# Optimization experiments

Measured on AMD Instinct MI355X. Metric: run time of the kernel, lower is better.

Reference implementation:

```python
import jax, jax.numpy as jnp
import numpy as np
from jax import lax

B, C_IN, H, W = 8, 64, 256, 256
HEADS, QD, U, VD = 4, 16, 1, 32  # heads, query_depth, intra_depth, v_depth = out_ch//heads
EPS = 1e-5  # BatchNorm eps (eval mode: running_mean=0, running_var=1)


def setup_inputs() -> dict:
    key = jax.random.key(0)
    ks = jax.random.split(key, 10)
    x = jax.random.normal(ks[0], (B, C_IN, H, W), dtype=jnp.float32)
    Wq = jax.random.normal(ks[1], (QD * HEADS, C_IN), dtype=jnp.float32) * 0.05
    gq = jax.random.normal(ks[2], (QD * HEADS,), dtype=jnp.float32) * 0.1 + 1.0
    bq = jax.random.normal(ks[3], (QD * HEADS,), dtype=jnp.float32) * 0.05
    Wk = jax.random.normal(ks[4], (QD * U, C_IN), dtype=jnp.float32) * 0.05
    Wv = jax.random.normal(ks[5], (VD * U, C_IN), dtype=jnp.float32) * 0.05
    gv = jax.random.normal(ks[6], (VD * U,), dtype=jnp.float32) * 0.1 + 1.0
    bv = jax.random.normal(ks[7], (VD * U,), dtype=jnp.float32) * 0.05
    Wp = jax.random.normal(ks[8], (QD, U, 1, 3, 3), dtype=jnp.float32) * 0.1  # Conv3d (1,3,3)
    bp = jax.random.normal(ks[9], (QD,), dtype=jnp.float32) * 0.05
    return {"x": x, "Wq": Wq, "gq": gq, "bq": bq, "Wk": Wk, "Wv": Wv,
            "gv": gv, "bv": bv, "Wp": Wp, "bp": bp}


def _bn_eval(y, gamma, beta):
    # BatchNorm in eval mode with running_mean=0, running_var=1
    s = gamma / jnp.sqrt(1.0 + EPS)
    return y * s[None, :, None, None] + beta[None, :, None, None]


def reference(x, Wq, gq, bq, Wk, Wv, gv, bv, Wp, bp):
    b, c, h, w = x.shape
    n = h * w
    # 1x1 convs as channel matmuls
    q = jnp.einsum('oc,bchw->bohw', Wq, x)
    q = _bn_eval(q, gq, bq).reshape(b, HEADS, QD, n)           # b h k n
    k = jnp.einsum('oc,bchw->bohw', Wk, x).reshape(b, U, QD, n)  # b u k m
    v = jnp.einsum('oc,bchw->bohw', Wv, x)
    v = _bn_eval(v, gv, bv).reshape(b, U, VD, n)               # b u v m
    k = jax.nn.softmax(k, axis=-1)
    # content lambda: global context
    lam_c = jnp.einsum('bukm,buvm->bkv', k, v)                 # b k v
    Yc = jnp.einsum('bhkn,bkv->bhvn', q, lam_c)
    # position lambda: 3D conv over (v-depth, h, w) with kernel (1,3,3)
    v_p = v.reshape(b, U, VD, h, w)                            # N C D H W (D = v-depth)
    lam_p = lax.conv_general_dilated(
        v_p, Wp, window_strides=(1, 1, 1),
        padding=[(0, 0), (1, 1), (1, 1)],
        dimension_numbers=('NCDHW', 'OIDHW', 'NCDHW'))
    lam_p = lam_p + bp[None, :, None, None, None]              # b k v h w
    Yp = jnp.einsum('bhkn,bkvn->bhvn', q, lam_p.reshape(b, QD, VD, n))
    Y = Yc + Yp                                                # b h v n
    return Y.reshape(b, HEADS * VD, h, w)
```

## Files before the change

### kernel.cpp

```cpp
#include <hip/hip_runtime.h>
#include <hip/hip_bf16.h>
#include <cstddef>

#define BB    8
#define CIN   64
#define HH    256
#define WW    256
#define NN    65536
#define NP    (BB*NN)
#define QC    64
#define KC    16
#define VC    32
#define HEADS 4
#define QD    16

#define WALL_OFF 0
#define BQ_OFF 7168
#define BV_OFF 7232
#define WP_OFF 7264
#define BP_OFF 7408
#define S_OFF  7424
#define M_OFF  7552
#define SMALL_END 11648
#define FLAG_OFF 12000
#define BF_BASE 65536

typedef __hip_bfloat16 bf16;
typedef __attribute__((ext_vector_type(8))) short short8;
typedef __attribute__((ext_vector_type(4))) short short4v;
typedef __attribute__((ext_vector_type(4))) float f32x4;

#define MFMA16(a, b, c) __builtin_amdgcn_mfma_f32_16x16x32_bf16((a), (b), (c), 0, 0, 0)

__device__ __forceinline__ short f2bf_s(float f) {
    bf16 h = (bf16)f;
    return __builtin_bit_cast(short, h);
}
__device__ __forceinline__ float bf2f(short u) {
    unsigned x = ((unsigned)(unsigned short)u) << 16;
    return __builtin_bit_cast(float, x);
}

__global__ void k_detect(const unsigned short* __restrict xu, int* __restrict flag) {
    if (threadIdx.x == 0 && blockIdx.x == 0) {
        int big = 0, zero = 0;
        for (int i = 0; i < 256; ++i) {
            unsigned short u = xu[i];
            int e = (u >> 7) & 0xFF;
            big  += (e >= 134);
            zero += (u == 0);
        }
        *flag = (big > 4 || zero > 64) ? 1 : 0;
    }
}

__device__ __forceinline__ float ldin(const void* p, int i, int isf) {
    return isf ? ((const float*)p)[i] : (float)(((const bf16*)p)[i]);
}

__global__ void k_prep(const void* __restrict wq, const void* __restrict gq,
                       const void* __restrict bq, const void* __restrict wk,
                       const void* __restrict wv, const void* __restrict gv,
                       const void* __restrict bv, const void* __restrict wp,
                       const void* __restrict bp, float* __restrict wf,
                       const int* __restrict flag) {
    int t = threadIdx.x;
    int isf = *flag;
    float rs = rsqrtf(1.0f + 1e-5f);
    for (int i = t; i < 4096; i += 256)
        wf[WALL_OFF + i] = ldin(wq, i, isf) * (ldin(gq, i>>6, isf) * rs);
    for (int i = t; i < 1024; i += 256)
        wf[WALL_OFF + 4096 + i] = ldin(wk, i, isf);
    for (int i = t; i < 2048; i += 256)
        wf[WALL_OFF + 5120 + i] = ldin(wv, i, isf) * (ldin(gv, i>>6, isf) * rs);
    for (int i = t; i < 64;   i += 256) wf[BQ_OFF+i] = ldin(bq, i, isf);
    for (int i = t; i < 32;   i += 256) wf[BV_OFF+i] = ldin(bv, i, isf);
    for (int i = t; i < 144;  i += 256) wf[WP_OFF+i] = ldin(wp, i, isf);
    for (int i = t; i < 16;   i += 256) wf[BP_OFF+i] = ldin(bp, i, isf);
    for (int i = t; i < SMALL_END - S_OFF; i += 256) wf[S_OFF + i] = 0.0f;
}

#define TPW 2
__global__ __launch_bounds__(256) void k_qkv(const void* __restrict x,
        const float* __restrict wf, const int* __restrict flag,
        bf16* __restrict qws2, bf16* __restrict ekws, bf16* __restrict vws) {
    const int lane = threadIdx.x & 63;
    const int m = lane & 15, g = lane >> 4;
    const int wave = blockIdx.x * 4 + (threadIdx.x >> 6);
    const int px0 = wave * (TPW * 16);
    const int b = px0 >> 16;
    const int n0 = px0 & 0xFFFF;
    const int isf = *flag;

    short8 a[7][2];
    #pragma unroll
    for (int mt = 0; mt < 7; ++mt)
        #pragma unroll
        for (int kh = 0; kh < 2; ++kh) {
            const float* wr = wf + WALL_OFF + (mt * 16 + m) * 64 + kh * 32 + g * 8;
            short8 t;
            #pragma unroll
            for (int i = 0; i < 8; ++i) t[i] = f2bf_s(wr[i]);
            a[mt][kh] = t;
        }

    f32x4 bias[7];
    #pragma unroll
    for (int mt = 0; mt < 4; ++mt)
        #pragma unroll
        for (int r = 0; r < 4; ++r) bias[mt][r] = wf[BQ_OFF + mt * 16 + g * 4 + r];
    #pragma unroll
    for (int r = 0; r < 4; ++r) bias[4][r] = 0.0f;
    #pragma unroll
    for (int mt = 5; mt < 7; ++mt)
        #pragma unroll
        for (int r = 0; r < 4; ++r) bias[mt][r] = wf[BV_OFF + (mt - 5) * 16 + g * 4 + r];

    #pragma unroll
    for (int it = 0; it < TPW; ++it) {
        const int n = n0 + it * 16 + m;
        const size_t p = (size_t)px0 + it * 16 + m;

        short8 bf0, bf1;
        if (isf) {
            const float* xp = (const float*)x + (size_t)b * CIN * NN
                            + (size_t)g * 8 * NN + n;
            #pragma unroll
            for (int i = 0; i < 8; ++i) bf0[i] = f2bf_s(xp[(size_t)i * NN]);
            #pragma unroll
            for (int i = 0; i < 8; ++i) bf1[i] = f2bf_s(xp[(size_t)(32 + i) * NN]);
        } else {
            const unsigned short* xp = (const unsigned short*)x + (size_t)b * CIN * NN
                                     + (size_t)g * 8 * NN + n;
            #pragma unroll
            for (int i = 0; i < 8; ++i) bf0[i] = (short)xp[(size_t)i * NN];
            #pragma unroll
            for (int i = 0; i < 8; ++i) bf1[i] = (short)xp[(size_t)(32 + i) * NN];
        }

        f32x4 acc[7];
        #pragma unroll
        for (int mt = 0; mt < 7; ++mt) {
            acc[mt] = MFMA16(a[mt][0], bf0, bias[mt]);
            acc[mt] = MFMA16(a[mt][1], bf1, acc[mt]);
        }

        bf16* qp = qws2 + p * 64;
        #pragma unroll
        for (int mt = 0; mt < 4; ++mt) {
            short4v pk;
            #pragma unroll
            for (int r = 0; r < 4; ++r) pk[r] = f2bf_s(acc[mt][r]);
            *(short4v*)(qp + mt * 16 + g * 4) = pk;
        }
        #pragma unroll
        for (int r = 0; r < 4; ++r)
            ekws[(size_t)(g * 4 + r) * NP + p] = (bf16)__expf(acc[4][r]);
        #pragma unroll
        for (int mt = 0; mt < 2; ++mt)
            #pragma unroll
            for (int r = 0; r < 4; ++r)
                vws[(size_t)(mt * 16 + g * 4 + r) * NP + p] = (bf16)acc[5 + mt][r];
    }
}

#define LCHUNK 256
__global__ __launch_bounds__(256) void k_lamc(const bf16* __restrict ekws,
        const bf16* __restrict vws, float* __restrict Sg, float* __restrict Mg) {
    __shared__ float MM[4][512];
    __shared__ float SS[4][16];
    const int b = blockIdx.y, chunk = blockIdx.x;
    const int t = threadIdx.x, w = t >> 6, lane = t & 63;
    const int m = lane & 15, g = lane >> 4;
    const size_t px0 = (size_t)b * NN + (size_t)chunk * LCHUNK + (size_t)w * 64;

    f32x4 acc0 = {0.f, 0.f, 0.f, 0.f}, acc1 = {0.f, 0.f, 0.f, 0.f};
    float s = 0.0f;
    #pragma unroll
    for (int st = 0; st < 2; ++st) {
        const size_t p = px0 + st * 32 + g * 8;
        short8 afr = *(const short8*)(ekws + (size_t)m * NP + p);
        short8 b0  = *(const short8*)(vws + (size_t)m * NP + p);
        short8 b1  = *(const short8*)(vws + (size_t)(16 + m) * NP + p);
        acc0 = MFMA16(afr, b0, acc0);
        acc1 = MFMA16(afr, b1, acc1);
        #pragma unroll
        for (int i = 0; i < 8; ++i) s += bf2f(afr[i]);
    }
    s += __shfl_xor(s, 16);
    s += __shfl_xor(s, 32);
    if (g == 0) SS[w][m] = s;
    #pragma unroll
    for (int r = 0; r < 4; ++r) {
        MM[w][(g * 4 + r) * 32 + m]      = acc0[r];
        MM[w][(g * 4 + r) * 32 + 16 + m] = acc1[r];
    }
    __syncthreads();
    for (int i = t; i < 512; i += 256) {
        float v4 = MM[0][i] + MM[1][i] + MM[2][i] + MM[3][i];
        atomicAdd(&Mg[b * 512 + i], v4);
    }
    if (t < 16) atomicAdd(&Sg[b * 16 + t], SS[0][t] + SS[1][t] + SS[2][t] + SS[3][t]);
}

__global__ __launch_bounds__(256) void k_out(const bf16* __restrict qws2,
        const bf16* __restrict vws, const float* __restrict wf,
        const float* __restrict Sg, const float* __restrict Mg,
        const int* __restrict flag, void* __restrict outv) {
    const int y = blockIdx.x >> 1, xh = blockIdx.x & 1, b = blockIdx.y;
    const int tid = threadIdx.x;
    const int pxl = tid & 127, hg = tid >> 7;
    const int px0 = xh * 128;
    const int isf = *flag;

    __shared__ float As[512];
    __shared__ float WPs[144];
    __shared__ unsigned short VS[32 * 3 * 144];

    for (int i = tid; i < 512; i += 256) {
        int k = i & 15, v = i >> 4;
        As[i] = Mg[b * 512 + k * 32 + v] / Sg[b * 16 + k] + wf[BP_OFF + k];
    }
    if (tid < 144) WPs[tid] = wf[WP_OFF + tid];

    #pragma unroll
    for (int kk = 0; kk < 7; ++kk) {
        int idx = tid + kk * 256;
        if (idx < 1728) {
            int c = idx / 54, rem = idx - c * 54;
            int j = rem / 18, i = rem - j * 18;
            int yy = y + j - 1;
            int x0 = px0 - 8 + i * 8;
            short8 val = {0, 0, 0, 0, 0, 0, 0, 0};
            if (yy >= 0 && yy < HH && x0 >= 0 && x0 <= WW - 8)
                val = *(const short8*)(vws + (size_t)c * NP + (size_t)b * NN
                                       + (size_t)yy * WW + x0);
            *(short8*)&VS[(c * 3 + j) * 144 + i * 8] = val;
        }
    }
    __syncthreads();

    const size_t pix = (size_t)b * NN + (size_t)y * WW + px0 + pxl;
    const short8* qrow = (const short8*)(qws2 + pix * 64) + hg * 4;
    float qf[32];
    #pragma unroll
    for (int j = 0; j < 4; ++j) {
        short8 qv = qrow[j];
        #pragma unroll
        for (int e = 0; e < 8; ++e) qf[j * 8 + e] = bf2f(qv[e]);
    }

    float g4[2][9];
    #pragma unroll
    for (int hl = 0; hl < 2; ++hl)
        #pragma unroll
        for (int tn = 0; tn < 9; ++tn) g4[hl][tn] = 0.0f;
    #pragma unroll
    for (int k = 0; k < 16; ++k)
        #pragma unroll
        for (int tn = 0; tn < 9; ++tn) {
            float w = WPs[k * 9 + tn];
            g4[0][tn] += qf[k] * w;
            g4[1][tn] += qf[16 + k] * w;
        }

    const size_t obase = ((size_t)(b * HEADS + hg * 2) * VC) * NN
                       + (size_t)y * WW + px0 + pxl;
    #pragma unroll 2
    for (int vc = 0; vc < VC; ++vc) {
        float vnf[9];
        const unsigned short* vb = &VS[vc * 3 * 144 + 7 + pxl];
        #pragma unroll
        for (int j = 0; j < 3; ++j)
            #pragma unroll
            for (int dx = 0; dx < 3; ++dx)
                vnf[j * 3 + dx] = bf2f((short)vb[j * 144 + dx]);
        float Ak[16];
        const f32x4* ap = (const f32x4*)&As[vc * 16];
        #pragma unroll
        for (int qq = 0; qq < 4; ++qq) {
            f32x4 a4 = ap[qq];
            #pragma unroll
            for (int e = 0; e < 4; ++e) Ak[qq * 4 + e] = a4[e];
        }
        #pragma unroll
        for (int hl = 0; hl < 2; ++hl) {
            float acc = 0.0f;
            #pragma unroll
            for (int k = 0; k < 16; ++k) acc += qf[hl * 16 + k] * Ak[k];
            #pragma unroll
            for (int tn = 0; tn < 9; ++tn) acc += g4[hl][tn] * vnf[tn];
            size_t idx2 = obase + ((size_t)hl * VC + vc) * NN;
            if (isf) ((float*)outv)[idx2] = acc;
            else     ((bf16*)outv)[idx2] = (bf16)acc;
        }
    }
}

extern "C" void kernel_launch(void* const* d_in, const int* in_sizes, int n_in,
                              void* d_out, int out_size, void* d_ws, size_t ws_size,
                              hipStream_t stream) {
    float* wf = (float*)d_ws;
    int* flag = (int*)wf + FLAG_OFF;
    bf16* qws2 = (bf16*)((char*)d_ws + BF_BASE);
    bf16* ekws = qws2 + (size_t)QC * NP;
    bf16* vws  = ekws + (size_t)KC * NP;

    k_detect<<<1, 64, 0, stream>>>((const unsigned short*)d_in[0], flag);
    k_prep<<<1, 256, 0, stream>>>(d_in[1], d_in[2], d_in[3], d_in[4], d_in[5],
                                  d_in[6], d_in[7], d_in[8], d_in[9], wf, flag);
    k_qkv<<<NP / 128, 256, 0, stream>>>(d_in[0], wf, flag, qws2, ekws, vws);
    k_lamc<<<dim3(NN / LCHUNK, BB), 256, 0, stream>>>(ekws, vws, wf + S_OFF, wf + M_OFF);
    k_out<<<dim3(2 * HH, BB), 256, 0, stream>>>(qws2, vws, wf, wf + S_OFF, wf + M_OFF,
                                                flag, d_out);
}
```

Baseline: 529.7 us.

## Replace lambda atomics with partial sums and reduce kernel, pre-swizzle weights

```diff
diff --git a/kernel.cpp b/kernel.cpp
--- a/kernel.cpp
+++ b/kernel.cpp
@@ -14,16 +14,16 @@
 #define HEADS 4
 #define QD    16
 
-#define WALL_OFF 0
 #define BQ_OFF 7168
 #define BV_OFF 7232
 #define WP_OFF 7264
 #define BP_OFF 7408
 #define S_OFF  7424
 #define M_OFF  7552
-#define SMALL_END 11648
 #define FLAG_OFF 12000
+#define WSW_BYTE 49152
 #define BF_BASE 65536
+#define NCHUNK 128
 
 typedef __hip_bfloat16 bf16;
 typedef __attribute__((ext_vector_type(8))) short short8;
@@ -67,20 +67,26 @@
     int t = threadIdx.x;
     int isf = *flag;
     float rs = rsqrtf(1.0f + 1e-5f);
-    for (int i = t; i < 4096; i += 256)
-        wf[WALL_OFF + i] = ldin(wq, i, isf) * (ldin(gq, i>>6, isf) * rs);
-    for (int i = t; i < 1024; i += 256)
-        wf[WALL_OFF + 4096 + i] = ldin(wk, i, isf);
-    for (int i = t; i < 2048; i += 256)
-        wf[WALL_OFF + 5120 + i] = ldin(wv, i, isf) * (ldin(gv, i>>6, isf) * rs);
-    for (int i = t; i < 64;   i += 256) wf[BQ_OFF+i] = ldin(bq, i, isf);
-    for (int i = t; i < 32;   i += 256) wf[BV_OFF+i] = ldin(bv, i, isf);
-    for (int i = t; i < 144;  i += 256) wf[WP_OFF+i] = ldin(wp, i, isf);
-    for (int i = t; i < 16;   i += 256) wf[BP_OFF+i] = ldin(bp, i, isf);
-    for (int i = t; i < SMALL_END - S_OFF; i += 256) wf[S_OFF + i] = 0.0f;
-}
-
-#define TPW 2
+    unsigned short* wsw = (unsigned short*)((char*)wf + WSW_BYTE);
+    for (int idx = t; idx < 7168; idx += 256) {
+        int i = idx & 7, lane = (idx >> 3) & 63, blk = idx >> 9;
+        int kh = blk & 1, mt = blk >> 1;
+        int m = lane & 15, g = lane >> 4;
+        int row = mt * 16 + m, col = kh * 32 + g * 8 + i;
+        float v;
+        if (row < 64)      v = ldin(wq, row * 64 + col, isf) * (ldin(gq, row, isf) * rs);
+        else if (row < 80) v = ldin(wk, (row - 64) * 64 + col, isf);
+        else               v = ldin(wv, (row - 80) * 64 + col, isf)
+                             * (ldin(gv, row - 80, isf) * rs);
+        wsw[idx] = (unsigned short)f2bf_s(v);
+    }
+    for (int i = t; i < 64;  i += 256) wf[BQ_OFF + i] = ldin(bq, i, isf);
+    for (int i = t; i < 32;  i += 256) wf[BV_OFF + i] = ldin(bv, i, isf);
+    for (int i = t; i < 144; i += 256) wf[WP_OFF + i] = ldin(wp, i, isf);
+    for (int i = t; i < 16;  i += 256) wf[BP_OFF + i] = ldin(bp, i, isf);
+}
+
+#define TPW 4
 __global__ __launch_bounds__(256) void k_qkv(const void* __restrict x,
         const float* __restrict wf, const int* __restrict flag,
         bf16* __restrict qws2, bf16* __restrict ekws, bf16* __restrict vws) {
@@ -92,29 +98,22 @@
     const int n0 = px0 & 0xFFFF;
     const int isf = *flag;
 
+    const unsigned short* wsw = (const unsigned short*)((const char*)wf + WSW_BYTE);
     short8 a[7][2];
     #pragma unroll
     for (int mt = 0; mt < 7; ++mt)
         #pragma unroll
-        for (int kh = 0; kh < 2; ++kh) {
-            const float* wr = wf + WALL_OFF + (mt * 16 + m) * 64 + kh * 32 + g * 8;
-            short8 t;
-            #pragma unroll
-            for (int i = 0; i < 8; ++i) t[i] = f2bf_s(wr[i]);
-            a[mt][kh] = t;
-        }
+        for (int kh = 0; kh < 2; ++kh)
+            a[mt][kh] = *(const short8*)(wsw + ((mt * 2 + kh) * 64 + lane) * 8);
 
     f32x4 bias[7];
     #pragma unroll
     for (int mt = 0; mt < 4; ++mt)
-        #pragma unroll
-        for (int r = 0; r < 4; ++r) bias[mt][r] = wf[BQ_OFF + mt * 16 + g * 4 + r];
-    #pragma unroll
-    for (int r = 0; r < 4; ++r) bias[4][r] = 0.0f;
+        bias[mt] = *(const f32x4*)(wf + BQ_OFF + mt * 16 + g * 4);
+    bias[4] = (f32x4){0.f, 0.f, 0.f, 0.f};
     #pragma unroll
     for (int mt = 5; mt < 7; ++mt)
-        #pragma unroll
-        for (int r = 0; r < 4; ++r) bias[mt][r] = wf[BV_OFF + (mt - 5) * 16 + g * 4 + r];
+        bias[mt] = *(const f32x4*)(wf + BV_OFF + (mt - 5) * 16 + g * 4);
 
     #pragma unroll
     for (int it = 0; it < TPW; ++it) {
@@ -164,20 +163,20 @@
     }
 }
 
-#define LCHUNK 256
 __global__ __launch_bounds__(256) void k_lamc(const bf16* __restrict ekws,
-        const bf16* __restrict vws, float* __restrict Sg, float* __restrict Mg) {
+        const bf16* __restrict vws, float* __restrict Mpart,
+        float* __restrict Spart) {
     __shared__ float MM[4][512];
     __shared__ float SS[4][16];
     const int b = blockIdx.y, chunk = blockIdx.x;
     const int t = threadIdx.x, w = t >> 6, lane = t & 63;
     const int m = lane & 15, g = lane >> 4;
-    const size_t px0 = (size_t)b * NN + (size_t)chunk * LCHUNK + (size_t)w * 64;
+    const size_t px0 = (size_t)b * NN + (size_t)chunk * 512 + (size_t)w * 128;
 
     f32x4 acc0 = {0.f, 0.f, 0.f, 0.f}, acc1 = {0.f, 0.f, 0.f, 0.f};
     float s = 0.0f;
     #pragma unroll
-    for (int st = 0; st < 2; ++st) {
+    for (int st = 0; st < 4; ++st) {
         const size_t p = px0 + st * 32 + g * 8;
         short8 afr = *(const short8*)(ekws + (size_t)m * NP + p);
         short8 b0  = *(const short8*)(vws + (size_t)m * NP + p);
@@ -196,11 +195,36 @@
         MM[w][(g * 4 + r) * 32 + 16 + m] = acc1[r];
     }
     __syncthreads();
-    for (int i = t; i < 512; i += 256) {
-        float v4 = MM[0][i] + MM[1][i] + MM[2][i] + MM[3][i];
-        atomicAdd(&Mg[b * 512 + i], v4);
-    }
-    if (t < 16) atomicAdd(&Sg[b * 16 + t], SS[0][t] + SS[1][t] + SS[2][t] + SS[3][t]);
+    for (int i = t; i < 512; i += 256)
+        Mpart[((size_t)b * NCHUNK + chunk) * 512 + i]
+            = MM[0][i] + MM[1][i] + MM[2][i] + MM[3][i];
+    if (t < 16)
+        Spart[((size_t)b * NCHUNK + chunk) * 16 + t]
+            = SS[0][t] + SS[1][t] + SS[2][t] + SS[3][t];
+}
+
+__global__ __launch_bounds__(256) void k_reduce(const float* __restrict Mpart,
+        const float* __restrict Spart, float* __restrict Mg, float* __restrict Sg) {
+    const int b = blockIdx.y, p = blockIdx.x, t = threadIdx.x;
+    __shared__ float R[256];
+    __shared__ float RS[128];
+    const int e = t & 63, c4 = t >> 6;
+    float a = 0.0f;
+    for (int c = c4; c < NCHUNK; c += 4)
+        a += Mpart[((size_t)b * NCHUNK + c) * 512 + p * 64 + e];
+    R[t] = a;
+    float s2 = 0.0f;
+    if (p == 0 && t < 128) {
+        int e2 = t & 15, c8 = t >> 4;
+        for (int c = c8; c < NCHUNK; c += 8)
+            s2 += Spart[((size_t)b * NCHUNK + c) * 16 + e2];
+    }
+    if (t < 128) RS[t] = s2;
+    __syncthreads();
+    if (t < 64) Mg[b * 512 + p * 64 + t] = R[t] + R[64 + t] + R[128 + t] + R[192 + t];
+    if (p == 0 && t < 16)
+        Sg[b * 16 + t] = RS[t] + RS[16 + t] + RS[32 + t] + RS[48 + t]
+                       + RS[64 + t] + RS[80 + t] + RS[96 + t] + RS[112 + t];
 }
 
 __global__ __launch_bounds__(256) void k_out(const bf16* __restrict qws2,
@@ -305,12 +329,15 @@
     bf16* qws2 = (bf16*)((char*)d_ws + BF_BASE);
     bf16* ekws = qws2 + (size_t)QC * NP;
     bf16* vws  = ekws + (size_t)KC * NP;
+    float* Mpart = (float*)((char*)d_ws + BF_BASE + (size_t)(QC + KC + VC) * NP * 2);
+    float* Spart = Mpart + (size_t)BB * NCHUNK * 512;
 
     k_detect<<<1, 64, 0, stream>>>((const unsigned short*)d_in[0], flag);
     k_prep<<<1, 256, 0, stream>>>(d_in[1], d_in[2], d_in[3], d_in[4], d_in[5],
                                   d_in[6], d_in[7], d_in[8], d_in[9], wf, flag);
-    k_qkv<<<NP / 128, 256, 0, stream>>>(d_in[0], wf, flag, qws2, ekws, vws);
-    k_lamc<<<dim3(NN / LCHUNK, BB), 256, 0, stream>>>(ekws, vws, wf + S_OFF, wf + M_OFF);
+    k_qkv<<<NP / 256, 256, 0, stream>>>(d_in[0], wf, flag, qws2, ekws, vws);
+    k_lamc<<<dim3(NCHUNK, BB), 256, 0, stream>>>(ekws, vws, Mpart, Spart);
+    k_reduce<<<dim3(8, BB), 256, 0, stream>>>(Mpart, Spart, wf + M_OFF, wf + S_OFF);
     k_out<<<dim3(2 * HH, BB), 256, 0, stream>>>(qws2, vws, wf, wf + S_OFF, wf + M_OFF,
                                                 flag, d_out);
 }
```

New measurement: 532.9 us. About the same (+0.6%).
